# Optimization experiments

Hardware: AMD Instinct MI355X
Metric: run time of the kernel (lower is better)

The kernel has to match this reference:

```python
import jax, jax.numpy as jnp
import numpy as np

K = 3          # kernel size
KF = K * K     # kernel field = 9
PAD = 1
STRIDE = 1


def _conv(x, w, b):
    y = jax.lax.conv_general_dilated(
        x, w, (STRIDE, STRIDE), [(PAD, PAD), (PAD, PAD)],
        dimension_numbers=('NCHW', 'OIHW', 'NCHW'))
    return y + b[None, :, None, None]


def _bilinear_gather(x, py, px):
    # x: [B,C,H,W]; py/px: [B,KF,Ho,Wo] float sampling coords (zero-pad outside)
    B, C, H, W = x.shape
    xf = x.reshape(B, C, H * W)
    y0 = jnp.floor(py)
    x0 = jnp.floor(px)

    def corner(yc, xc):
        wy = 1.0 - jnp.abs(py - yc)
        wx = 1.0 - jnp.abs(px - xc)
        valid = (yc >= 0) & (yc <= H - 1) & (xc >= 0) & (xc <= W - 1)
        yi = jnp.clip(yc, 0, H - 1).astype(jnp.int32)
        xi = jnp.clip(xc, 0, W - 1).astype(jnp.int32)
        idx = (yi * W + xi).reshape(B, -1)               # [B, KF*Ho*Wo]
        v = jax.vmap(lambda f, i: f[:, i])(xf, idx)      # [B, C, KF*Ho*Wo]
        wgt = (wy * wx * valid.astype(x.dtype)).reshape(B, 1, -1)
        return v * wgt

    return (corner(y0, x0) + corner(y0, x0 + 1) +
            corner(y0 + 1, x0) + corner(y0 + 1, x0 + 1))  # [B,C,KF*Ho*Wo]


def _deform_conv(x, offset, mask, w, b):
    # modulated deformable conv v2 (mmcv offset layout: [y,x] interleaved per kernel pt)
    B, C, H, W = x.shape
    Ho, Wo = mask.shape[2], mask.shape[3]
    kh, kw = jnp.meshgrid(jnp.arange(K), jnp.arange(K), indexing='ij')
    kh = kh.reshape(-1).astype(x.dtype)   # [KF]
    kw = kw.reshape(-1).astype(x.dtype)
    base_y = (jnp.arange(Ho) * STRIDE - PAD).astype(x.dtype)
    base_x = (jnp.arange(Wo) * STRIDE - PAD).astype(x.dtype)
    off = offset.reshape(B, KF, 2, Ho, Wo)
    py = base_y[None, None, :, None] + kh[None, :, None, None] + off[:, :, 0]
    px = base_x[None, None, None, :] + kw[None, :, None, None] + off[:, :, 1]
    val = _bilinear_gather(x, py, px).reshape(B, C, KF, Ho, Wo)
    val = val * mask[:, None]                             # modulate
    out = jnp.einsum('bckhw,ock->bohw', val, w.reshape(w.shape[0], C, KF))
    return out + b[None, :, None, None]


def setup_inputs() -> dict:
    key = jax.random.key(0)
    k1, k2, k3 = jax.random.split(key, 3)
    B, C, H, W = 8, 64, 128, 128
    x = jax.random.normal(k1, (B, C, H, W), dtype=jnp.float32)
    w_om = jax.random.normal(k2, (3 * KF, C, K, K), dtype=jnp.float32) * 0.02
    b_om = jnp.zeros((3 * KF,), dtype=jnp.float32)
    w_dc = jax.random.normal(k3, (64, C, K, K), dtype=jnp.float32) * 0.05
    b_dc = jnp.zeros((64,), dtype=jnp.float32)
    return {"x": x, "w_om": w_om, "b_om": b_om, "w_dc": w_dc, "b_dc": b_dc}


def reference(x, w_om, b_om, w_dc, b_dc):
    om = _conv(x, w_om, b_om)                 # [B, 3*KF, H, W]
    offset = om[:, :2 * KF]
    mask = 2.0 * jax.nn.sigmoid(om[:, 2 * KF:])
    return _deform_conv(x, offset, mask, w_dc, b_dc)
```

## Files before the change

### kernel.cpp

```cpp
#include <hip/hip_runtime.h>
#include <cmath>

#define IH 128
#define IW 128
#define NB 8

typedef __attribute__((ext_vector_type(8))) short bf16x8;
typedef __attribute__((ext_vector_type(4))) float f32x4;

#define OFFM_OFF 0
#define XT_OFF   3538944
#define WTDC_OFF (3538944 + 4194304)
#define WTOM_OFF (3538944 + 4194304 + 18432)

__device__ __forceinline__ unsigned short f32_to_bf16(float f) {
    unsigned int u = __float_as_uint(f);
    u += 0x7fffu + ((u >> 16) & 1u);
    return (unsigned short)(u >> 16);
}

__global__ void transpose_weights(const float* __restrict__ w_dc,
                                  const float* __restrict__ w_om,
                                  unsigned short* __restrict__ wt_dc16,
                                  unsigned short* __restrict__ wt_om16) {
    int idx = blockIdx.x * blockDim.x + threadIdx.x;
    if (idx < 9 * 64 * 64) {
        int k = idx >> 12;
        int o = (idx >> 6) & 63;
        int c = idx & 63;
        wt_dc16[idx] = f32_to_bf16(w_dc[(o * 64 + c) * 9 + k]);
    }
    if (idx < 9 * 32 * 64) {
        int k = idx >> 11;
        int o = (idx >> 6) & 31;
        int c = idx & 63;
        wt_om16[idx] = (o < 27) ? f32_to_bf16(w_om[(o * 64 + c) * 9 + k])
                                : (unsigned short)0;
    }
}

__global__ __launch_bounds__(256) void transpose_x(
        const float* __restrict__ x, unsigned short* __restrict__ xT) {
    __shared__ float t[64 * 65];
    const int tid = threadIdx.x;
    const int blk = blockIdx.x;
    const int b = blk >> 8;
    const int rem = blk & 255;
    const int h = rem >> 1;
    const int w0 = (rem & 1) << 6;

    for (int i = tid; i < 4096; i += 256) {
        const int c = i >> 6;
        const int w = i & 63;
        t[w * 65 + c] = x[(((size_t)(b * 64 + c)) << 14) + (h << 7) + w0 + w];
    }
    __syncthreads();
    const int c2 = (tid & 31) * 2;
    ushort2* dst = (ushort2*)(xT + (((size_t)b << 20)) + ((size_t)((h << 7) + w0)) * 64 + c2);
#pragma unroll
    for (int p = 0; p < 8; ++p) {
        const int w = (tid >> 5) + p * 8;
        ushort2 u;
        u.x = f32_to_bf16(t[w * 65 + c2]);
        u.y = f32_to_bf16(t[w * 65 + c2 + 1]);
        dst[(size_t)w * 32] = u;
    }
}

__global__ __launch_bounds__(256) void conv_om_mfma(
        const unsigned short* __restrict__ xT,
        const float* __restrict__ b_om,
        const unsigned short* __restrict__ wt_om16,
        float* __restrict__ offm) {
    __shared__ __align__(16) unsigned short win[198 * 72];
    __shared__ __align__(16) unsigned short wks[32 * 72];

    const int tid = threadIdx.x;
    const int b = blockIdx.x >> 8;
    const int rem = blockIdx.x & 255;
    const int h = rem >> 1;
    const int w0 = (rem & 1) << 6;

    for (int idx = tid; idx < 1584; idx += 256) {
        const int pos = idx >> 3;
        const int part = idx & 7;
        const int r = pos / 66;
        const int xx = pos - r * 66;
        const int y = h + r - 1;
        const int xg = w0 + xx - 1;
        uint4 v = make_uint4(0u, 0u, 0u, 0u);
        if (y >= 0 && y < IH && xg >= 0 && xg < IW)
            v = *(const uint4*)(xT + (((size_t)b << 20) + (((y << 7) + xg) << 6) + (part << 3)));
        *(uint4*)&win[pos * 72 + part * 8] = v;
    }

    const int wid = tid >> 6;
    const int lane = tid & 63;
    const int ln15 = lane & 15;
    const int quad = lane >> 4;

    f32x4 acc[2] = {{0.f, 0.f, 0.f, 0.f}, {0.f, 0.f, 0.f, 0.f}};

    for (int k = 0; k < 9; ++k) {
        __syncthreads();
        {
            const int o = tid >> 3;
            const int part = tid & 7;
            *(uint4*)&wks[o * 72 + part * 8] =
                *(const uint4*)(wt_om16 + (k << 11) + (o << 6) + (part << 3));
        }
        __syncthreads();
        const int kh = k / 3;
        const int kw = k - kh * 3;
        const int posb = kh * 66 + wid * 16 + ln15 + kw;
#pragma unroll
        for (int ch = 0; ch < 2; ++ch) {
            const int c = (ch << 5) + (quad << 3);
            const bf16x8 a  = *(const bf16x8*)&win[posb * 72 + c];
            const bf16x8 b0 = *(const bf16x8*)&wks[ln15 * 72 + c];
            const bf16x8 b1 = *(const bf16x8*)&wks[(16 + ln15) * 72 + c];
            acc[0] = __builtin_amdgcn_mfma_f32_16x16x32_bf16(a, b0, acc[0], 0, 0, 0);
            acc[1] = __builtin_amdgcn_mfma_f32_16x16x32_bf16(a, b1, acc[1], 0, 0, 0);
        }
    }

    const int px0 = wid * 16 + quad * 4;
#pragma unroll
    for (int ot = 0; ot < 2; ++ot) {
        const int o = ot * 16 + ln15;
        if (o >= 27) continue;
        const float bias = b_om[o];
        float4 r;
        r.x = acc[ot][0] + bias;
        r.y = acc[ot][1] + bias;
        r.z = acc[ot][2] + bias;
        r.w = acc[ot][3] + bias;
        if (o >= 18) {
            r.x = 2.0f / (1.0f + __expf(-r.x));
            r.y = 2.0f / (1.0f + __expf(-r.y));
            r.z = 2.0f / (1.0f + __expf(-r.z));
            r.w = 2.0f / (1.0f + __expf(-r.w));
        }
        *(float4*)&offm[(((size_t)(b * 27 + o)) << 14) + (h << 7) + w0 + px0] = r;
    }
}

__device__ __forceinline__ void corner_acc(const unsigned short* __restrict__ xb,
                                           int pos, int cg, float wgt, float* v) {
    const uint4* p = (const uint4*)(xb + ((size_t)pos << 6) + (cg << 4));
    const uint4 a = p[0];
    const uint4 b = p[1];
    unsigned int u[8] = {a.x, a.y, a.z, a.w, b.x, b.y, b.z, b.w};
#pragma unroll
    for (int i = 0; i < 8; ++i) {
        v[2 * i]     += wgt * __uint_as_float(u[i] << 16);
        v[2 * i + 1] += wgt * __uint_as_float(u[i] & 0xffff0000u);
    }
}

__global__ __launch_bounds__(256) void deform_mfma(
        const unsigned short* __restrict__ xT,
        const float* __restrict__ b_dc,
        const float* __restrict__ offm,
        const unsigned short* __restrict__ wt_dc16,
        float* __restrict__ out) {
    __shared__ __align__(16) float offs[27 * 64];
    __shared__ __align__(16) unsigned short vm[64 * 72];
    __shared__ __align__(16) unsigned short wks[64 * 72];

    const int tid = threadIdx.x;
    const int b = blockIdx.x >> 8;
    const int rem = blockIdx.x & 255;
    const int h = rem >> 1;
    const int w0 = (rem & 1) << 6;

    for (int i = tid; i < 1728; i += 256) {
        const int ch = i >> 6;
        const int px = i & 63;
        offs[i] = offm[(((size_t)(b * 27 + ch)) << 14) + (h << 7) + w0 + px];
    }

    const int px = tid & 63;
    const int cg = tid >> 6;
    const int wid = tid >> 6;
    const int lane = tid & 63;
    const int ln15 = lane & 15;
    const int quad = lane >> 4;
    const int pt0 = (wid >> 1) << 1;
    const int ot0 = (wid & 1) << 1;

    const unsigned short* xb = xT + ((size_t)b << 20);

    f32x4 acc[2][2];
#pragma unroll
    for (int i = 0; i < 2; ++i)
#pragma unroll
        for (int j = 0; j < 2; ++j) acc[i][j] = (f32x4){0.f, 0.f, 0.f, 0.f};

    for (int k = 0; k < 9; ++k) {
        __syncthreads();
        for (int idx = tid; idx < 512; idx += 256) {
            const int o = idx >> 3;
            const int part = idx & 7;
            *(uint4*)&wks[o * 72 + part * 8] =
                *(const uint4*)(wt_dc16 + (k << 12) + (o << 6) + (part << 3));
        }
        const float offy = offs[(k << 1) * 64 + px];
        const float offx = offs[((k << 1) + 1) * 64 + px];
        const float msk = offs[(18 + k) * 64 + px];
        const int kh = k / 3;
        const int kw = k - kh * 3;
        const float py = (float)(h + kh - 1) + offy;
        const float pxf = (float)(w0 + px + kw - 1) + offx;
        const float y0f = floorf(py);
        const float x0f = floorf(pxf);
        const float fy = py - y0f;
        const float fx = pxf - x0f;
        const float wy0 = 1.0f - fy, wx0 = 1.0f - fx;
        const float vy0 = (y0f >= 0.0f && y0f <= 127.0f) ? 1.0f : 0.0f;
        const float vy1 = (y0f >= -1.0f && y0f <= 126.0f) ? 1.0f : 0.0f;
        const float vx0 = (x0f >= 0.0f && x0f <= 127.0f) ? 1.0f : 0.0f;
        const float vx1 = (x0f >= -1.0f && x0f <= 126.0f) ? 1.0f : 0.0f;
        const float w00 = wy0 * wx0 * vy0 * vx0;
        const float w01 = wy0 * fx  * vy0 * vx1;
        const float w10 = fy  * wx0 * vy1 * vx0;
        const float w11 = fy  * fx  * vy1 * vx1;
        const int y0i = min(max((int)y0f, 0), 127);
        const int y1i = min(max((int)y0f + 1, 0), 127);
        const int x0i = min(max((int)x0f, 0), 127);
        const int x1i = min(max((int)x0f + 1, 0), 127);

        float v[16];
#pragma unroll
        for (int i = 0; i < 16; ++i) v[i] = 0.0f;
        corner_acc(xb, (y0i << 7) + x0i, cg, w00, v);
        corner_acc(xb, (y0i << 7) + x1i, cg, w01, v);
        corner_acc(xb, (y1i << 7) + x0i, cg, w10, v);
        corner_acc(xb, (y1i << 7) + x1i, cg, w11, v);

        unsigned int pk[8];
#pragma unroll
        for (int i = 0; i < 8; ++i) {
            const unsigned int lo = f32_to_bf16(v[2 * i] * msk);
            const unsigned int hi = f32_to_bf16(v[2 * i + 1] * msk);
            pk[i] = lo | (hi << 16);
        }
        uint4* vdst = (uint4*)&vm[px * 72 + cg * 16];
        vdst[0] = make_uint4(pk[0], pk[1], pk[2], pk[3]);
        vdst[1] = make_uint4(pk[4], pk[5], pk[6], pk[7]);

        __syncthreads();
#pragma unroll
        for (int ch = 0; ch < 2; ++ch) {
            const int c = (ch << 5) + (quad << 3);
            const bf16x8 a0 = *(const bf16x8*)&vm[(pt0 * 16 + ln15) * 72 + c];
            const bf16x8 a1 = *(const bf16x8*)&vm[((pt0 + 1) * 16 + ln15) * 72 + c];
            const bf16x8 b0 = *(const bf16x8*)&wks[(ot0 * 16 + ln15) * 72 + c];
            const bf16x8 b1 = *(const bf16x8*)&wks[((ot0 + 1) * 16 + ln15) * 72 + c];
            acc[0][0] = __builtin_amdgcn_mfma_f32_16x16x32_bf16(a0, b0, acc[0][0], 0, 0, 0);
            acc[0][1] = __builtin_amdgcn_mfma_f32_16x16x32_bf16(a0, b1, acc[0][1], 0, 0, 0);
            acc[1][0] = __builtin_amdgcn_mfma_f32_16x16x32_bf16(a1, b0, acc[1][0], 0, 0, 0);
            acc[1][1] = __builtin_amdgcn_mfma_f32_16x16x32_bf16(a1, b1, acc[1][1], 0, 0, 0);
        }
    }

#pragma unroll
    for (int pt = 0; pt < 2; ++pt) {
#pragma unroll
        for (int ot = 0; ot < 2; ++ot) {
            const int o = (ot0 + ot) * 16 + ln15;
            const float bias = b_dc[o];
            const int px0 = (pt0 + pt) * 16 + quad * 4;
            float4 r;
            r.x = acc[pt][ot][0] + bias;
            r.y = acc[pt][ot][1] + bias;
            r.z = acc[pt][ot][2] + bias;
            r.w = acc[pt][ot][3] + bias;
            *(float4*)&out[(((size_t)(b * 64 + o)) << 14) + (h << 7) + w0 + px0] = r;
        }
    }
}

extern "C" void kernel_launch(void* const* d_in, const int* in_sizes, int n_in,
                              void* d_out, int out_size, void* d_ws, size_t ws_size,
                              hipStream_t stream) {
    const float* x    = (const float*)d_in[0];
    const float* w_om = (const float*)d_in[1];
    const float* b_om = (const float*)d_in[2];
    const float* w_dc = (const float*)d_in[3];
    const float* b_dc = (const float*)d_in[4];
    float* out = (float*)d_out;
    float* ws  = (float*)d_ws;

    float* offm = ws + OFFM_OFF;
    unsigned short* xT      = (unsigned short*)(ws + XT_OFF);
    unsigned short* wt_dc16 = (unsigned short*)(ws + WTDC_OFF);
    unsigned short* wt_om16 = (unsigned short*)(ws + WTOM_OFF);

    transpose_weights<<<144, 256, 0, stream>>>(w_dc, w_om, wt_dc16, wt_om16);
    transpose_x<<<NB * IH * 2, 256, 0, stream>>>(x, xT);
    conv_om_mfma<<<NB * IH * 2, 256, 0, stream>>>(xT, b_om, wt_om16, offm);
    deform_mfma<<<NB * IH * 2, 256, 0, stream>>>(xT, b_dc, offm, wt_dc16, out);
}
```

Baseline: 194.8 us.

## Drop shared memory staging; give each wave an independent 16-pixel tile

Both the offset/mask conv and the deformable conv now assign one 16-pixel tile to each wavefront. MFMA operands are loaded straight from global memory into registers, replacing the previous shared-memory windows, weight staging and per-tap block barriers. In the deform kernel each lane samples a full 16-channel slice for its own pixel, so the bilinear result feeds the MFMA A operand without an LDS round-trip. This removes synchronisation and LDS traffic, at the cost of redundant global or L2 loads for weights and halo pixels across waves, and no shared reuse.

```diff
diff --git a/kernel.cpp b/kernel.cpp
--- a/kernel.cpp
+++ b/kernel.cpp
@@ -7,6 +7,8 @@
 
 typedef __attribute__((ext_vector_type(8))) short bf16x8;
 typedef __attribute__((ext_vector_type(4))) float f32x4;
+
+union U4B8 { uint4 u; bf16x8 h; };
 
 #define OFFM_OFF 0
 #define XT_OFF   3538944
@@ -72,62 +74,49 @@
         const float* __restrict__ b_om,
         const unsigned short* __restrict__ wt_om16,
         float* __restrict__ offm) {
-    __shared__ __align__(16) unsigned short win[198 * 72];
-    __shared__ __align__(16) unsigned short wks[32 * 72];
-
     const int tid = threadIdx.x;
-    const int b = blockIdx.x >> 8;
-    const int rem = blockIdx.x & 255;
-    const int h = rem >> 1;
-    const int w0 = (rem & 1) << 6;
-
-    for (int idx = tid; idx < 1584; idx += 256) {
-        const int pos = idx >> 3;
-        const int part = idx & 7;
-        const int r = pos / 66;
-        const int xx = pos - r * 66;
-        const int y = h + r - 1;
-        const int xg = w0 + xx - 1;
-        uint4 v = make_uint4(0u, 0u, 0u, 0u);
-        if (y >= 0 && y < IH && xg >= 0 && xg < IW)
-            v = *(const uint4*)(xT + (((size_t)b << 20) + (((y << 7) + xg) << 6) + (part << 3)));
-        *(uint4*)&win[pos * 72 + part * 8] = v;
-    }
-
-    const int wid = tid >> 6;
+    const int t = (blockIdx.x << 2) + (tid >> 6);
+    const int b = t >> 10;
+    const int rem = t & 1023;
+    const int h = rem >> 3;
+    const int w0 = (rem & 7) << 4;
     const int lane = tid & 63;
     const int ln15 = lane & 15;
     const int quad = lane >> 4;
 
+    const unsigned short* xb = xT + ((size_t)b << 20);
+
     f32x4 acc[2] = {{0.f, 0.f, 0.f, 0.f}, {0.f, 0.f, 0.f, 0.f}};
 
+#pragma unroll
     for (int k = 0; k < 9; ++k) {
-        __syncthreads();
-        {
-            const int o = tid >> 3;
-            const int part = tid & 7;
-            *(uint4*)&wks[o * 72 + part * 8] =
-                *(const uint4*)(wt_om16 + (k << 11) + (o << 6) + (part << 3));
-        }
-        __syncthreads();
         const int kh = k / 3;
         const int kw = k - kh * 3;
-        const int posb = kh * 66 + wid * 16 + ln15 + kw;
-#pragma unroll
-        for (int ch = 0; ch < 2; ++ch) {
-            const int c = (ch << 5) + (quad << 3);
-            const bf16x8 a  = *(const bf16x8*)&win[posb * 72 + c];
-            const bf16x8 b0 = *(const bf16x8*)&wks[ln15 * 72 + c];
-            const bf16x8 b1 = *(const bf16x8*)&wks[(16 + ln15) * 72 + c];
-            acc[0] = __builtin_amdgcn_mfma_f32_16x16x32_bf16(a, b0, acc[0], 0, 0, 0);
-            acc[1] = __builtin_amdgcn_mfma_f32_16x16x32_bf16(a, b1, acc[1], 0, 0, 0);
-        }
-    }
-
-    const int px0 = wid * 16 + quad * 4;
+        const int y = h + kh - 1;
+        const int xx = w0 + ln15 + kw - 1;
+        U4B8 a0, a1;
+        a0.u = make_uint4(0u, 0u, 0u, 0u);
+        a1.u = make_uint4(0u, 0u, 0u, 0u);
+        if (y >= 0 && y < IH && xx >= 0 && xx < IW) {
+            const unsigned short* p = xb + (((size_t)((y << 7) + xx)) << 6) + (quad << 3);
+            a0.u = *(const uint4*)p;
+            a1.u = *(const uint4*)(p + 32);
+        }
+        const unsigned short* wk = wt_om16 + (k << 11) + (quad << 3);
+#pragma unroll
+        for (int ot = 0; ot < 2; ++ot) {
+            U4B8 b0, b1;
+            const unsigned short* base = wk + (((ot << 4) + ln15) << 6);
+            b0.u = *(const uint4*)base;
+            b1.u = *(const uint4*)(base + 32);
+            acc[ot] = __builtin_amdgcn_mfma_f32_16x16x32_bf16(a0.h, b0.h, acc[ot], 0, 0, 0);
+            acc[ot] = __builtin_amdgcn_mfma_f32_16x16x32_bf16(a1.h, b1.h, acc[ot], 0, 0, 0);
+        }
+    }
+
 #pragma unroll
     for (int ot = 0; ot < 2; ++ot) {
-        const int o = ot * 16 + ln15;
+        const int o = (ot << 4) + ln15;
         if (o >= 27) continue;
         const float bias = b_om[o];
         float4 r;
@@ -141,16 +130,15 @@
             r.z = 2.0f / (1.0f + __expf(-r.z));
             r.w = 2.0f / (1.0f + __expf(-r.w));
         }
-        *(float4*)&offm[(((size_t)(b * 27 + o)) << 14) + (h << 7) + w0 + px0] = r;
-    }
-}
-
-__device__ __forceinline__ void corner_acc(const unsigned short* __restrict__ xb,
-                                           int pos, int cg, float wgt, float* v) {
-    const uint4* p = (const uint4*)(xb + ((size_t)pos << 6) + (cg << 4));
-    const uint4 a = p[0];
-    const uint4 b = p[1];
-    unsigned int u[8] = {a.x, a.y, a.z, a.w, b.x, b.y, b.z, b.w};
+        *(float4*)&offm[(((size_t)(b * 27 + o)) << 14) + (h << 7) + w0 + (quad << 2)] = r;
+    }
+}
+
+__device__ __forceinline__ void corner2(const unsigned short* __restrict__ p,
+                                        float wgt, float* v) {
+    const uint4 a = *(const uint4*)p;
+    const uint4 c = *(const uint4*)(p + 32);
+    unsigned int u[8] = {a.x, a.y, a.z, a.w, c.x, c.y, c.z, c.w};
 #pragma unroll
     for (int i = 0; i < 8; ++i) {
         v[2 * i]     += wgt * __uint_as_float(u[i] << 16);
@@ -164,54 +152,32 @@
         const float* __restrict__ offm,
         const unsigned short* __restrict__ wt_dc16,
         float* __restrict__ out) {
-    __shared__ __align__(16) float offs[27 * 64];
-    __shared__ __align__(16) unsigned short vm[64 * 72];
-    __shared__ __align__(16) unsigned short wks[64 * 72];
-
     const int tid = threadIdx.x;
-    const int b = blockIdx.x >> 8;
-    const int rem = blockIdx.x & 255;
-    const int h = rem >> 1;
-    const int w0 = (rem & 1) << 6;
-
-    for (int i = tid; i < 1728; i += 256) {
-        const int ch = i >> 6;
-        const int px = i & 63;
-        offs[i] = offm[(((size_t)(b * 27 + ch)) << 14) + (h << 7) + w0 + px];
-    }
-
-    const int px = tid & 63;
-    const int cg = tid >> 6;
-    const int wid = tid >> 6;
+    const int t = (blockIdx.x << 2) + (tid >> 6);
+    const int b = t >> 10;
+    const int rem = t & 1023;
+    const int h = rem >> 3;
+    const int w0 = (rem & 7) << 4;
     const int lane = tid & 63;
     const int ln15 = lane & 15;
     const int quad = lane >> 4;
-    const int pt0 = (wid >> 1) << 1;
-    const int ot0 = (wid & 1) << 1;
 
     const unsigned short* xb = xT + ((size_t)b << 20);
-
-    f32x4 acc[2][2];
-#pragma unroll
-    for (int i = 0; i < 2; ++i)
-#pragma unroll
-        for (int j = 0; j < 2; ++j) acc[i][j] = (f32x4){0.f, 0.f, 0.f, 0.f};
-
+    const float* ofb = offm + (((size_t)(b * 27)) << 14) + (h << 7) + w0 + ln15;
+
+    f32x4 acc[4];
+#pragma unroll
+    for (int i = 0; i < 4; ++i) acc[i] = (f32x4){0.f, 0.f, 0.f, 0.f};
+
+#pragma unroll
     for (int k = 0; k < 9; ++k) {
-        __syncthreads();
-        for (int idx = tid; idx < 512; idx += 256) {
-            const int o = idx >> 3;
-            const int part = idx & 7;
-            *(uint4*)&wks[o * 72 + part * 8] =
-                *(const uint4*)(wt_dc16 + (k << 12) + (o << 6) + (part << 3));
-        }
-        const float offy = offs[(k << 1) * 64 + px];
-        const float offx = offs[((k << 1) + 1) * 64 + px];
-        const float msk = offs[(18 + k) * 64 + px];
+        const float offy = ofb[((size_t)(2 * k)) << 14];
+        const float offx = ofb[((size_t)(2 * k + 1)) << 14];
+        const float msk  = ofb[((size_t)(18 + k)) << 14];
         const int kh = k / 3;
         const int kw = k - kh * 3;
-        const float py = (float)(h + kh - 1) + offy;
-        const float pxf = (float)(w0 + px + kw - 1) + offx;
+        const float py  = (float)(h + kh - 1) + offy;
+        const float pxf = (float)(w0 + ln15 + kw - 1) + offx;
         const float y0f = floorf(py);
         const float x0f = floorf(pxf);
         const float fy = py - y0f;
@@ -233,11 +199,13 @@
         float v[16];
 #pragma unroll
         for (int i = 0; i < 16; ++i) v[i] = 0.0f;
-        corner_acc(xb, (y0i << 7) + x0i, cg, w00, v);
-        corner_acc(xb, (y0i << 7) + x1i, cg, w01, v);
-        corner_acc(xb, (y1i << 7) + x0i, cg, w10, v);
-        corner_acc(xb, (y1i << 7) + x1i, cg, w11, v);
-
+        const int cofs = quad << 3;
+        corner2(xb + ((((size_t)((y0i << 7) + x0i)) << 6) + cofs), w00, v);
+        corner2(xb + ((((size_t)((y0i << 7) + x1i)) << 6) + cofs), w01, v);
+        corner2(xb + ((((size_t)((y1i << 7) + x0i)) << 6) + cofs), w10, v);
+        corner2(xb + ((((size_t)((y1i << 7) + x1i)) << 6) + cofs), w11, v);
+
+        U4B8 a0, a1;
         unsigned int pk[8];
 #pragma unroll
         for (int i = 0; i < 8; ++i) {
@@ -245,39 +213,31 @@
             const unsigned int hi = f32_to_bf16(v[2 * i + 1] * msk);
             pk[i] = lo | (hi << 16);
         }
-        uint4* vdst = (uint4*)&vm[px * 72 + cg * 16];
-        vdst[0] = make_uint4(pk[0], pk[1], pk[2], pk[3]);
-        vdst[1] = make_uint4(pk[4], pk[5], pk[6], pk[7]);
-
-        __syncthreads();
-#pragma unroll
-        for (int ch = 0; ch < 2; ++ch) {
-            const int c = (ch << 5) + (quad << 3);
-            const bf16x8 a0 = *(const bf16x8*)&vm[(pt0 * 16 + ln15) * 72 + c];
-            const bf16x8 a1 = *(const bf16x8*)&vm[((pt0 + 1) * 16 + ln15) * 72 + c];
-            const bf16x8 b0 = *(const bf16x8*)&wks[(ot0 * 16 + ln15) * 72 + c];
-            const bf16x8 b1 = *(const bf16x8*)&wks[((ot0 + 1) * 16 + ln15) * 72 + c];
-            acc[0][0] = __builtin_amdgcn_mfma_f32_16x16x32_bf16(a0, b0, acc[0][0], 0, 0, 0);
-            acc[0][1] = __builtin_amdgcn_mfma_f32_16x16x32_bf16(a0, b1, acc[0][1], 0, 0, 0);
-            acc[1][0] = __builtin_amdgcn_mfma_f32_16x16x32_bf16(a1, b0, acc[1][0], 0, 0, 0);
-            acc[1][1] = __builtin_amdgcn_mfma_f32_16x16x32_bf16(a1, b1, acc[1][1], 0, 0, 0);
-        }
-    }
-
-#pragma unroll
-    for (int pt = 0; pt < 2; ++pt) {
-#pragma unroll
-        for (int ot = 0; ot < 2; ++ot) {
-            const int o = (ot0 + ot) * 16 + ln15;
-            const float bias = b_dc[o];
-            const int px0 = (pt0 + pt) * 16 + quad * 4;
-            float4 r;
-            r.x = acc[pt][ot][0] + bias;
-            r.y = acc[pt][ot][1] + bias;
-            r.z = acc[pt][ot][2] + bias;
-            r.w = acc[pt][ot][3] + bias;
-            *(float4*)&out[(((size_t)(b * 64 + o)) << 14) + (h << 7) + w0 + px0] = r;
-        }
+        a0.u = make_uint4(pk[0], pk[1], pk[2], pk[3]);
+        a1.u = make_uint4(pk[4], pk[5], pk[6], pk[7]);
+
+        const unsigned short* wk = wt_dc16 + (k << 12) + (quad << 3);
+#pragma unroll
+        for (int ot = 0; ot < 4; ++ot) {
+            U4B8 b0, b1;
+            const unsigned short* base = wk + (((ot << 4) + ln15) << 6);
+            b0.u = *(const uint4*)base;
+            b1.u = *(const uint4*)(base + 32);
+            acc[ot] = __builtin_amdgcn_mfma_f32_16x16x32_bf16(a0.h, b0.h, acc[ot], 0, 0, 0);
+            acc[ot] = __builtin_amdgcn_mfma_f32_16x16x32_bf16(a1.h, b1.h, acc[ot], 0, 0, 0);
+        }
+    }
+
+#pragma unroll
+    for (int ot = 0; ot < 4; ++ot) {
+        const int o = (ot << 4) + ln15;
+        const float bias = b_dc[o];
+        float4 r;
+        r.x = acc[ot][0] + bias;
+        r.y = acc[ot][1] + bias;
+        r.z = acc[ot][2] + bias;
+        r.w = acc[ot][3] + bias;
+        *(float4*)&out[(((size_t)(b * 64 + o)) << 14) + (h << 7) + w0 + (quad << 2)] = r;
     }
 }
 
@@ -297,8 +257,10 @@
     unsigned short* wt_dc16 = (unsigned short*)(ws + WTDC_OFF);
     unsigned short* wt_om16 = (unsigned short*)(ws + WTOM_OFF);
 
+    const int n_tiles_blocks = NB * IH * (IW / 16) / 4;
+
     transpose_weights<<<144, 256, 0, stream>>>(w_dc, w_om, wt_dc16, wt_om16);
     transpose_x<<<NB * IH * 2, 256, 0, stream>>>(x, xT);
-    conv_om_mfma<<<NB * IH * 2, 256, 0, stream>>>(xT, b_om, wt_om16, offm);
-    deform_mfma<<<NB * IH * 2, 256, 0, stream>>>(xT, b_dc, offm, wt_dc16, out);
-}
+    conv_om_mfma<<<n_tiles_blocks, 256, 0, stream>>>(xT, b_om, wt_om16, offm);
+    deform_mfma<<<n_tiles_blocks, 256, 0, stream>>>(xT, b_dc, offm, wt_dc16, out);
+}
```

New measurement: 265.6 us. 1.36x slower.
